# Optimization experiments

Hardware: AMD Instinct MI355X
Metric: run time of the kernel (lower is better)

Reference implementation:

```python
import jax, jax.numpy as jnp
import numpy as np
import math

SQRT32 = math.sqrt(32.0)


def _l2norm(x, eps=1e-12):
    # matches torch.nn.functional.normalize(dim=-1): x / max(||x||, eps)
    n = jnp.linalg.norm(x, axis=-1, keepdims=True)
    return x / jnp.maximum(n, eps)


def setup_inputs() -> dict:
    key = jax.random.key(0)
    k1, k2 = jax.random.split(key)
    z = jax.random.normal(k1, (8, 256, 32, 32), dtype=jnp.float32)
    # trunc_normal_(std=0.02) init approximated by scaled normal
    embed_weight = jax.random.normal(k2, (16384, 256), dtype=jnp.float32) * 0.02
    return {"z": z, "embed_weight": embed_weight}


def reference(z, embed_weight):
    # z: [b, d, h, w] channel-first -> pack to [b*h*w, d]
    b, d, h, w = z.shape
    zf = jnp.transpose(z, (0, 2, 3, 1)).reshape(-1, d)  # [N, d]

    # l2_norm=True, no predefined codebook: distance = -z @ normalize(E)^T
    ew = _l2norm(embed_weight)                          # [K, d]
    dist = -(zf @ ew.T)                                 # [N, K]
    min_encoding_indices = jnp.argmin(dist, axis=1)     # [N]

    # gather UNnormalized embedding rows, then normalize (as in source)
    z_q = _l2norm(embed_weight[min_encoding_indices])   # [N, d]

    # straight-through estimator
    z_q = zf + jax.lax.stop_gradient(z_q - zf)

    loss = jnp.zeros((1,), dtype=z.dtype)

    # unpack to [b, h, w, d]
    zq_bhwd = z_q.reshape(b, h, w, d)
    # torch .long() truncates toward zero; astype(int) does the same
    bit_indices = (zq_bhwd * SQRT32).astype(jnp.int32) + 4
    zq_out = jnp.transpose(zq_bhwd, (0, 3, 1, 2))       # [b, d, h, w]

    return zq_out, min_encoding_indices, bit_indices, loss
```

## Files before the change

### kernel.cpp

```cpp
#include <hip/hip_runtime.h>
#include <math.h>

#define D      256
#define K      16384
#define NPTS   8192
#define DELTA  0.2f
#define LCAP   2048
#define MAXCAP 4000000u

#define O_IDX  2097152
#define O_BIT  2105344
#define O_LOSS 4202496

typedef __attribute__((ext_vector_type(8))) short bf16x8;
typedef __attribute__((ext_vector_type(4))) float f32x4;
typedef unsigned long long u64;

__device__ __forceinline__ unsigned f2s(float f) {
    unsigned u = __float_as_uint(f);
    return (u & 0x80000000u) ? ~u : (u | 0x80000000u);
}
__device__ __forceinline__ float s2f(unsigned s) {
    return __uint_as_float((s & 0x80000000u) ? (s & 0x7fffffffu) : ~s);
}
__device__ __forceinline__ unsigned short f2bf(float f) {
    unsigned u = __float_as_uint(f);
    u += 0x7fffu + ((u >> 16) & 1u);
    return (unsigned short)(u >> 16);
}

__device__ __forceinline__ void gload16(const unsigned short* g, unsigned short* l) {
    __builtin_amdgcn_global_load_lds(
        (const __attribute__((address_space(1))) unsigned int*)g,
        (__attribute__((address_space(3))) unsigned int*)l, 16, 0, 0);
}

__device__ __forceinline__ unsigned lds_off(const void* p) {
    return (unsigned)(size_t)(const __attribute__((address_space(3))) void*)p;
}


__global__ __launch_bounds__(256) void prep(const float* __restrict__ E,
                                            const float* __restrict__ z,
                                            float* __restrict__ den,
                                            unsigned short* __restrict__ ewbT,
                                            unsigned short* __restrict__ zfbT,
                                            float* __restrict__ zf32,
                                            unsigned* __restrict__ gmax,
                                            u64* __restrict__ keys,
                                            unsigned* __restrict__ cnt) {
    const int blk = blockIdx.x, tid = threadIdx.x;
    if (blk < 512) {
        const int lane = tid & 63, wave = tid >> 6;
        if (blk < 32)        gmax[blk * 256 + tid] = 0u;
        else if (blk < 64)   keys[(blk - 32) * 256 + tid] = 0ull;
        else if (blk == 64 && tid < 2) cnt[tid] = 0u;
        #pragma unroll
        for (int j = 0; j < 8; ++j) {
            const int row = blk * 32 + wave * 8 + j;
            const float4 v = *(const float4*)(E + (size_t)row * D + lane * 4);
            float ss = v.x * v.x + v.y * v.y + v.z * v.z + v.w * v.w;
            #pragma unroll
            for (int o = 1; o < 64; o <<= 1) ss += __shfl_xor(ss, o);
            const float dn = fmaxf(sqrtf(ss), 1e-12f);
            const unsigned lo = (unsigned)f2bf(v.x / dn) | ((unsigned)f2bf(v.y / dn) << 16);
            const unsigned hi = (unsigned)f2bf(v.z / dn) | ((unsigned)f2bf(v.w / dn) << 16);
            *(uint2*)(ewbT + ((size_t)(lane >> 1) * K + row) * 8 + (lane & 1) * 4)
                = make_uint2(lo, hi);
            if (lane == 0) den[row] = dn;
        }
    } else {
        const int bi = blk - 512;
        const int b = bi >> 4, hw0 = (bi & 15) * 64;
        __shared__ float t[64][65];
        for (int dc = 0; dc < D; dc += 64) {
            #pragma unroll
            for (int it = 0; it < 16; ++it) {
                const int idx = it * 256 + tid;
                const int dl = idx >> 6, hw = idx & 63;
                t[dl][hw] = z[(size_t)(b * 256 + dc + dl) * 1024 + hw0 + hw];
            }
            __syncthreads();
            #pragma unroll
            for (int it = 0; it < 16; ++it) {
                const int idx = it * 256 + tid;
                const int pl = idx >> 6, dl = idx & 63;
                const float v = t[dl][pl];
                const int p = b * 1024 + hw0 + pl, k = dc + dl;
                zfbT[((size_t)(k >> 3) * NPTS + p) * 8 + (k & 7)] = f2bf(v);
                zf32[(size_t)p * D + k] = v;
            }
            __syncthreads();
        }
    }
}


#define SBAR  __builtin_amdgcn_sched_barrier(0);
#define BARR  __builtin_amdgcn_s_barrier();
#define VMC(N) asm volatile("s_waitcnt vmcnt(" N ")");
#define LGKM_SB  asm volatile("s_waitcnt lgkmcnt(0)"); __builtin_amdgcn_sched_barrier(0);

#define STG_A(slot, t, kk)                                                          \
    do {                                                                            \
        const int cA1_ = (kk) * 4 + hi_, cA2_ = (kk) * 4 + 2 + hi_;                 \
        gload16(zfbT + ((size_t)((t) * 8 + cA1_) * NPTS + m0 + (th_ ^ (cA1_ << 1))) * 8, \
                &sA[slot][cA1_][th_][0]);                                           \
        gload16(zfbT + ((size_t)((t) * 8 + cA2_) * NPTS + m0 + (th_ ^ (cA2_ << 1))) * 8, \
                &sA[slot][cA2_][th_][0]);                                           \
    } while (0)

#define STG_B(slot, t, kk)                                                          \
    do {                                                                            \
        const int cB1_ = (kk) * 4 + hi_, cB2_ = (kk) * 4 + 2 + hi_;                 \
        gload16(ewbT + ((size_t)((t) * 8 + cB1_) * K + n0 + (th_ ^ (cB1_ << 1))) * 8, \
                &sB[slot][cB1_][th_][0]);                                           \
        gload16(ewbT + ((size_t)((t) * 8 + cB2_) * K + n0 + (th_ ^ (cB2_ << 1))) * 8, \
                &sB[slot][cB2_][th_][0]);                                           \
    } while (0)

#define RD_A(slot, kO, mg)                                                          \
    do {                                                                            \
        const unsigned a__ = sAb_ + (unsigned)((slot) * 32768 + (mg) * 1024) + (kO);\
        asm volatile("ds_read_b128 %0, %1"            : "=v"(af_[0]) : "v"(a__));   \
        asm volatile("ds_read_b128 %0, %1 offset:256" : "=v"(af_[1]) : "v"(a__));   \
        asm volatile("ds_read_b128 %0, %1 offset:512" : "=v"(af_[2]) : "v"(a__));   \
        asm volatile("ds_read_b128 %0, %1 offset:768" : "=v"(af_[3]) : "v"(a__));   \
    } while (0)

#define RD_B(slot, kO)                                                              \
    do {                                                                            \
        const unsigned b__ = sBb_ + (unsigned)((slot) * 32768) + (kO);              \
        asm volatile("ds_read_b128 %0, %1"            : "=v"(bf_[0]) : "v"(b__));   \
        asm volatile("ds_read_b128 %0, %1 offset:256" : "=v"(bf_[1]) : "v"(b__));   \
        asm volatile("ds_read_b128 %0, %1 offset:512" : "=v"(bf_[2]) : "v"(b__));   \
        asm volatile("ds_read_b128 %0, %1 offset:768" : "=v"(bf_[3]) : "v"(b__));   \
    } while (0)

#define MF(mg)                                                                      \
    do {                                                                            \
        __builtin_amdgcn_s_setprio(1);                                              \
        _Pragma("unroll")                                                           \
        for (int j_ = 0; j_ < 4; ++j_)                                              \
            _Pragma("unroll")                                                       \
            for (int nt_ = 0; nt_ < 4; ++nt_)                                       \
                acc[(mg) * 4 + j_][nt_] = __builtin_amdgcn_mfma_f32_16x16x32_bf16(  \
                    af_[j_], bf_[nt_], acc[(mg) * 4 + j_][nt_], 0, 0, 0);           \
        __builtin_amdgcn_s_setprio(0);                                              \
    } while (0)

#define KTILE(slot, SA0, SB0, SA1, SB1, V1, V2)                                     \
    RD_A(slot, aOff0_, 0); RD_B(slot, bOff0_); SA0; SBAR BARR LGKM_SB MF(0); SBAR BARR SBAR \
    RD_A(slot, aOff0_, 1);                     SB0; SBAR BARR LGKM_SB MF(1); SBAR VMC(V1) BARR SBAR \
    RD_A(slot, aOff1_, 0); RD_B(slot, bOff1_); SA1; SBAR BARR LGKM_SB MF(0); SBAR BARR SBAR \
    RD_A(slot, aOff1_, 1);                     SB1; SBAR BARR LGKM_SB MF(1); SBAR V2 BARR SBAR

#define GEMM_CORE()                                                                 \
    __shared__ unsigned short sA[2][8][256][8];                                     \
    __shared__ unsigned short sB[2][8][256][8];                                     \
    f32x4 acc[8][4];                                                                \
    _Pragma("unroll")                                                               \
    for (int i_ = 0; i_ < 8; ++i_)                                                  \
        _Pragma("unroll")                                                           \
        for (int j_ = 0; j_ < 4; ++j_) acc[i_][j_] = (f32x4){0.f, 0.f, 0.f, 0.f};   \
    bf16x8 af_[4], bf_[4];                                                          \
    const int th_ = tid & 255, hi_ = tid >> 8;                                      \
    const int aRow_ = wm * 128 + col, bRow_ = wn * 64 + col;                        \
    const unsigned sAb_ = lds_off(&sA[0][0][0][0]);                                 \
    const unsigned sBb_ = lds_off(&sB[0][0][0][0]);                                 \
    const int ck0_ = quad, ck1_ = 4 + quad;                                         \
    const unsigned aOff0_ = (unsigned)((ck0_ * 256 + (aRow_ ^ (ck0_ << 1))) * 16);  \
    const unsigned aOff1_ = (unsigned)((ck1_ * 256 + (aRow_ ^ (ck1_ << 1))) * 16);  \
    const unsigned bOff0_ = (unsigned)((ck0_ * 256 + (bRow_ ^ (ck0_ << 1))) * 16);  \
    const unsigned bOff1_ = (unsigned)((ck1_ * 256 + (bRow_ ^ (ck1_ << 1))) * 16);  \
    STG_A(0, 0, 0); STG_B(0, 0, 0); STG_A(0, 0, 1); STG_B(0, 0, 1);                 \
    SBAR VMC("4") BARR SBAR                                                         \
    KTILE(0, STG_A(1, 1, 0), STG_B(1, 1, 0), STG_A(1, 1, 1), STG_B(1, 1, 1), "4", VMC("4")) \
    KTILE(1, STG_A(0, 2, 0), STG_B(0, 2, 0), STG_A(0, 2, 1), STG_B(0, 2, 1), "4", VMC("4")) \
    KTILE(0, STG_A(1, 3, 0), STG_B(1, 3, 0), STG_A(1, 3, 1), STG_B(1, 3, 1), "4", VMC("4")) \
    KTILE(1, , , , , "0", )

#define CAND_APPEND(e)                                                              \
    do {                                                                            \
        const u64 am_ = __builtin_amdgcn_read_exec();                               \
        const unsigned n_ = (unsigned)__popcll(am_);                                \
        const unsigned rk_ = (unsigned)__popcll(am_ & ((1ull << lane) - 1));        \
        unsigned base_ = 0;                                                         \
        if (rk_ == 0) base_ = atomicAdd(cnt, n_);                                   \
        base_ = (unsigned)__builtin_amdgcn_readfirstlane((int)base_);               \
        const unsigned g_ = base_ + rk_;                                            \
        if (g_ < cap) cand[g_] = (e);                                               \
    } while (0)

#define XCD_DECODE(NT0)                                                             \
    const unsigned bid_ = blockIdx.x;                                               \
    const unsigned j_ = bid_ >> 3;                                                  \
    const int m0 = (int)(((bid_ & 7u) << 2) | (j_ & 3u)) * 256;                     \
    const int n0 = (NT0) + (int)(j_ >> 2) * 256;

__global__ __launch_bounds__(512, 2) void score_seed(const unsigned short* __restrict__ zfbT,
                                                     const unsigned short* __restrict__ ewbT,
                                                     unsigned* __restrict__ gmax,
                                                     u64* __restrict__ cand,
                                                     unsigned* __restrict__ cnt,
                                                     unsigned cap) {
    __shared__ unsigned thrS[256];
    __shared__ u64 lbuf[LCAP];
    __shared__ unsigned lcount, lbase;

    const int tid = threadIdx.x, lane = tid & 63, wave = tid >> 6;
    const int quad = lane >> 4, col = lane & 15;
    const int wm = wave >> 2, wn = wave & 3;
    XCD_DECODE(0)
    const int shsrc = lane & 48;

    if (tid < 256) thrS[tid] = 0u;
    if (tid == 0) lcount = 0u;

    GEMM_CORE()
    __syncthreads();

    float red[8][4];
    #pragma unroll
    for (int mt = 0; mt < 8; ++mt)
        #pragma unroll
        for (int r = 0; r < 4; ++r)
            red[mt][r] = fmaxf(fmaxf(acc[mt][0][r], acc[mt][1][r]),
                               fmaxf(acc[mt][2][r], acc[mt][3][r]));
    #pragma unroll
    for (int off = 1; off < 16; off <<= 1)
        #pragma unroll
        for (int mt = 0; mt < 8; ++mt)
            #pragma unroll
            for (int r = 0; r < 4; ++r)
                red[mt][r] = fmaxf(red[mt][r], __shfl_xor(red[mt][r], off));
    #pragma unroll
    for (int mt = 0; mt < 8; ++mt)
        #pragma unroll
        for (int r = 0; r < 4; ++r) {
            const int pl = wm * 128 + mt * 16 + quad * 4 + r;
            unsigned cur = 0;
            if (col == 0) {
                const unsigned enc = f2s(red[mt][r]);
                const unsigned old = atomicMax(&thrS[pl], enc);
                cur = old > enc ? old : enc;
            }
            cur = (unsigned)__shfl((int)cur, shsrc);
            red[mt][r] = s2f(cur) - DELTA;
        }

    const int ncode0 = n0 + wn * 64 + col;
    #pragma unroll
    for (int mt = 0; mt < 8; ++mt) {
        #pragma unroll
        for (int r = 0; r < 4; ++r) {
            const float tp = red[mt][r];
            const unsigned pt = m0 + wm * 128 + mt * 16 + quad * 4 + r;
            #pragma unroll
            for (int nt = 0; nt < 4; ++nt) {
                const float v = acc[mt][nt][r];
                if (v >= tp) {
                    const unsigned slot = atomicAdd(&lcount, 1u);
                    const u64 e = ((u64)((pt << 14) | (unsigned)(ncode0 + nt * 16)) << 32)
                                  | f2s(v);
                    if (slot < LCAP) lbuf[slot] = e;
                    else CAND_APPEND(e);
                }
            }
        }
    }

    __syncthreads();
    if (tid < 256) atomicMax(&gmax[m0 + tid], thrS[tid]);
    const unsigned m_ = lcount < LCAP ? lcount : LCAP;
    if (tid == 0) lbase = atomicAdd(cnt, m_);
    __syncthreads();
    for (unsigned i = tid; i < m_; i += 512) {
        const unsigned g = lbase + i;
        if (g < cap) cand[g] = lbuf[i];
    }
}

__global__ __launch_bounds__(512, 2) void score_main(const unsigned short* __restrict__ zfbT,
                                                     const unsigned short* __restrict__ ewbT,
                                                     const unsigned* __restrict__ gmax,
                                                     u64* __restrict__ cand,
                                                     unsigned* __restrict__ cnt,
                                                     unsigned cap) {
    __shared__ float thrL[256];
    __shared__ u64 lbuf[LCAP];
    __shared__ unsigned lcount, lbase;

    const int tid = threadIdx.x, lane = tid & 63, wave = tid >> 6;
    const int quad = lane >> 4, col = lane & 15;
    const int wm = wave >> 2, wn = wave & 3;
    XCD_DECODE(2048)

    if (tid < 256) thrL[tid] = s2f(gmax[m0 + tid]) - DELTA;
    if (tid == 0) lcount = 0u;

    GEMM_CORE()
    __syncthreads();

    const int ncode0 = n0 + wn * 64 + col;
    #pragma unroll
    for (int mt = 0; mt < 8; ++mt) {
        #pragma unroll
        for (int r = 0; r < 4; ++r) {
            const int pl = wm * 128 + mt * 16 + quad * 4 + r;
            const float tp = thrL[pl];
            #pragma unroll
            for (int nt = 0; nt < 4; ++nt) {
                const float v = acc[mt][nt][r];
                if (v >= tp) {
                    const unsigned slot = atomicAdd(&lcount, 1u);
                    const u64 e = ((u64)(((unsigned)pl + m0) << 14 | (unsigned)(ncode0 + nt * 16)) << 32)
                                  | f2s(v);
                    if (slot < LCAP) lbuf[slot] = e;
                    else CAND_APPEND(e);
                }
            }
        }
    }

    __syncthreads();
    const unsigned m_ = lcount < LCAP ? lcount : LCAP;
    if (tid == 0) lbase = atomicAdd(cnt, m_);
    __syncthreads();
    for (unsigned i = tid; i < m_; i += 512) {
        const unsigned g = lbase + i;
        if (g < cap) cand[g] = lbuf[i];
    }
}

__global__ __launch_bounds__(256) void cand_max(const u64* __restrict__ cand,
                                                const unsigned* __restrict__ cnt,
                                                unsigned* __restrict__ gmax,
                                                unsigned cap) {
    const unsigned total = min(cnt[0], cap);
    const unsigned stride = gridDim.x * 256;
    for (unsigned i = blockIdx.x * 256 + threadIdx.x; i < total; i += stride) {
        const u64 e = cand[i];
        atomicMax(&gmax[(unsigned)(e >> 46)], (unsigned)(e & 0xffffffffull));
    }
}

__global__ __launch_bounds__(256) void rescore(const float* __restrict__ zf32,
                                               const float* __restrict__ E,
                                               const float* __restrict__ den,
                                               const unsigned* __restrict__ gmax,
                                               const u64* __restrict__ cand,
                                               const unsigned* __restrict__ cnt,
                                               u64* __restrict__ keys,
                                               unsigned cap) {
    const unsigned total = min(cnt[0], cap);
    const int lane = threadIdx.x & 63;
    const unsigned w = (blockIdx.x * 256 + threadIdx.x) >> 6;
    const unsigned nw = gridDim.x * 4;
    for (unsigned base = w * 64; base < total; base += nw * 64) {
        const unsigned i = base + lane;
        u64 e = 0;
        bool keep = false;
        if (i < total) {
            e = cand[i];
            const int p = (int)(e >> 46);
            keep = (s2f((unsigned)(e & 0xffffffffull)) >= s2f(gmax[p]) - DELTA);
        }
        u64 mask = __ballot(keep);
        while (mask) {
            const int src = __ffsll((long long)mask) - 1;
            mask &= mask - 1;
            const unsigned pc = (unsigned)__shfl((int)(unsigned)(e >> 32), src);
            const int p = pc >> 14, c = pc & 16383;
            const float dinv = 1.0f / den[c];
            const float4 a = *(const float4*)(zf32 + (size_t)p * D + lane * 4);
            const float4 b = *(const float4*)(E + (size_t)c * D + lane * 4);
            float sv = fmaf(a.x, b.x * dinv, fmaf(a.y, b.y * dinv,
                       fmaf(a.z, b.z * dinv, a.w * (b.w * dinv))));
            #pragma unroll
            for (int o = 1; o < 64; o <<= 1) sv += __shfl_xor(sv, o);
            if (lane == 0)
                atomicMax(keys + p, ((u64)f2s(sv) << 32) | (unsigned)(16383 - c));
        }
    }
}

__global__ __launch_bounds__(256) void finalize(const float* __restrict__ E,
                                                const float* __restrict__ den,
                                                const u64* __restrict__ keys,
                                                float* __restrict__ out) {
    __shared__ float t[32][257];
    __shared__ int sIdx[32];
    __shared__ float sDen[32];
    const int tid = threadIdx.x;
    const int n0 = blockIdx.x * 32;
    if (tid < 32) {
        const u64 key = keys[n0 + tid];
        const int idx = 16383 - (int)(unsigned)(key & 0xffffffffull);
        sIdx[tid] = idx;
        sDen[tid] = den[idx];
        out[O_IDX + n0 + tid] = (float)idx;
    }
    __syncthreads();
    const float S = 5.65685424949238019520675489683895f;
    #pragma unroll 4
    for (int i = 0; i < 32; ++i) {
        const float v = E[(size_t)sIdx[i] * D + tid] / sDen[i];
        t[i][tid] = v;
        out[O_BIT + (size_t)(n0 + i) * D + tid] = (float)((int)(v * S) + 4);
    }
    __syncthreads();
    const int b = n0 >> 10, hw0 = n0 & 1023;
    const int hwl = tid & 31, cg = tid >> 5;
    #pragma unroll 4
    for (int cc = 0; cc < 32; ++cc) {
        const int c = cc * 8 + cg;
        out[(size_t)(b * 256 + c) * 1024 + hw0 + hwl] = t[hwl][c];
    }
    if (n0 == 0 && tid == 0) out[O_LOSS] = 0.0f;
}

extern "C" void kernel_launch(void* const* d_in, const int* in_sizes, int n_in,
                              void* d_out, int out_size, void* d_ws, size_t ws_size,
                              hipStream_t stream) {
    const float* z = (const float*)d_in[0];
    const float* E = (const float*)d_in[1];
    float* out = (float*)d_out;

    char* w = (char*)d_ws;
    unsigned short* ewbT = (unsigned short*)w;  w += (size_t)K * D * 2;
    unsigned short* zfbT = (unsigned short*)w;  w += (size_t)NPTS * D * 2;
    float*          zf32 = (float*)w;           w += (size_t)NPTS * D * 4;
    u64*            keys = (u64*)w;             w += (size_t)NPTS * 8;
    float*          den  = (float*)w;           w += (size_t)K * 4;
    unsigned*       gmax = (unsigned*)w;        w += (size_t)NPTS * 4;
    unsigned*       cnt  = (unsigned*)w;        w += 256;
    u64*            cand = (u64*)w;
    const size_t fixed = (size_t)(w - (char*)d_ws);
    const size_t avail = ws_size > fixed ? (ws_size - fixed) / 8 : 0;
    const unsigned cap = (unsigned)(avail < (size_t)MAXCAP ? avail : (size_t)MAXCAP);

    prep<<<640, 256, 0, stream>>>(E, z, den, ewbT, zfbT, zf32, gmax, keys, cnt);

    score_seed<<<256, 512, 0, stream>>>(zfbT, ewbT, gmax, cand, cnt, cap);
    score_main<<<1792, 512, 0, stream>>>(zfbT, ewbT, gmax, cand, cnt, cap);

    cand_max<<<256, 256, 0, stream>>>(cand, cnt, gmax, cap);
    rescore<<<1024, 256, 0, stream>>>(zf32, E, den, gmax, cand, cnt, keys, cap);
    finalize<<<NPTS / 32, 256, 0, stream>>>(E, den, keys, out);
}
```

Baseline: 232.9 us.

## Double-buffer MFMA register fragments to overlap LDS reads with matrix math

Splits the A/B register fragments into two sets (a0/a1, b0/b1) and reorganizes the K-tile loop into four phases that issue LDS reads for the next fragment before running MFMAs on the current one. Partial lgkmcnt waits replace full drains, and fewer barriers are used per phase, so LDS latency is meant to hide behind MFMA work. The cost is more VGPRs for the extra fragments, which may lower occupancy, and a more delicate ordering of waits and barriers across buffer slots.

After: 281.3 us. 1.21x slower.

```diff
diff --git a/kernel.cpp b/kernel.cpp
--- a/kernel.cpp
+++ b/kernel.cpp
@@ -99,7 +99,7 @@
 #define SBAR  __builtin_amdgcn_sched_barrier(0);
 #define BARR  __builtin_amdgcn_s_barrier();
 #define VMC(N) asm volatile("s_waitcnt vmcnt(" N ")");
-#define LGKM_SB  asm volatile("s_waitcnt lgkmcnt(0)"); __builtin_amdgcn_sched_barrier(0);
+#define LGKM(N) asm volatile("s_waitcnt lgkmcnt(" N ")"); __builtin_amdgcn_sched_barrier(0);
 
 #define STG_A(slot, t, kk)                                                          \
     do {                                                                            \
@@ -119,25 +119,25 @@
                 &sB[slot][cB2_][th_][0]);                                           \
     } while (0)
 
-#define RD_A(slot, kO, mg)                                                          \
+#define RDA(dst, slot, kO, mg)                                                      \
     do {                                                                            \
         const unsigned a__ = sAb_ + (unsigned)((slot) * 32768 + (mg) * 1024) + (kO);\
-        asm volatile("ds_read_b128 %0, %1"            : "=v"(af_[0]) : "v"(a__));   \
-        asm volatile("ds_read_b128 %0, %1 offset:256" : "=v"(af_[1]) : "v"(a__));   \
-        asm volatile("ds_read_b128 %0, %1 offset:512" : "=v"(af_[2]) : "v"(a__));   \
-        asm volatile("ds_read_b128 %0, %1 offset:768" : "=v"(af_[3]) : "v"(a__));   \
-    } while (0)
-
-#define RD_B(slot, kO)                                                              \
+        asm volatile("ds_read_b128 %0, %1"            : "=v"(dst[0]) : "v"(a__));   \
+        asm volatile("ds_read_b128 %0, %1 offset:256" : "=v"(dst[1]) : "v"(a__));   \
+        asm volatile("ds_read_b128 %0, %1 offset:512" : "=v"(dst[2]) : "v"(a__));   \
+        asm volatile("ds_read_b128 %0, %1 offset:768" : "=v"(dst[3]) : "v"(a__));   \
+    } while (0)
+
+#define RDB(dst, slot, kO)                                                          \
     do {                                                                            \
         const unsigned b__ = sBb_ + (unsigned)((slot) * 32768) + (kO);              \
-        asm volatile("ds_read_b128 %0, %1"            : "=v"(bf_[0]) : "v"(b__));   \
-        asm volatile("ds_read_b128 %0, %1 offset:256" : "=v"(bf_[1]) : "v"(b__));   \
-        asm volatile("ds_read_b128 %0, %1 offset:512" : "=v"(bf_[2]) : "v"(b__));   \
-        asm volatile("ds_read_b128 %0, %1 offset:768" : "=v"(bf_[3]) : "v"(b__));   \
-    } while (0)
-
-#define MF(mg)                                                                      \
+        asm volatile("ds_read_b128 %0, %1"            : "=v"(dst[0]) : "v"(b__));   \
+        asm volatile("ds_read_b128 %0, %1 offset:256" : "=v"(dst[1]) : "v"(b__));   \
+        asm volatile("ds_read_b128 %0, %1 offset:512" : "=v"(dst[2]) : "v"(b__));   \
+        asm volatile("ds_read_b128 %0, %1 offset:768" : "=v"(dst[3]) : "v"(b__));   \
+    } while (0)
+
+#define MF2(mg, A, B)                                                               \
     do {                                                                            \
         __builtin_amdgcn_s_setprio(1);                                              \
         _Pragma("unroll")                                                           \
@@ -145,15 +145,21 @@
             _Pragma("unroll")                                                       \
             for (int nt_ = 0; nt_ < 4; ++nt_)                                       \
                 acc[(mg) * 4 + j_][nt_] = __builtin_amdgcn_mfma_f32_16x16x32_bf16(  \
-                    af_[j_], bf_[nt_], acc[(mg) * 4 + j_][nt_], 0, 0, 0);           \
+                    A[j_], B[nt_], acc[(mg) * 4 + j_][nt_], 0, 0, 0);               \
         __builtin_amdgcn_s_setprio(0);                                              \
     } while (0)
 
-#define KTILE(slot, SA0, SB0, SA1, SB1, V1, V2)                                     \
-    RD_A(slot, aOff0_, 0); RD_B(slot, bOff0_); SA0; SBAR BARR LGKM_SB MF(0); SBAR BARR SBAR \
-    RD_A(slot, aOff0_, 1);                     SB0; SBAR BARR LGKM_SB MF(1); SBAR VMC(V1) BARR SBAR \
-    RD_A(slot, aOff1_, 0); RD_B(slot, bOff1_); SA1; SBAR BARR LGKM_SB MF(0); SBAR BARR SBAR \
-    RD_A(slot, aOff1_, 1);                     SB1; SBAR BARR LGKM_SB MF(1); SBAR V2 BARR SBAR
+#define PH0(s, STG)                                                                 \
+    RDA(a1_, s, aOff0_, 1); STG; SBAR LGKM("4") MF2(0, a0_, b0_); SBAR
+#define PH1(s, STG, VM)                                                             \
+    SBAR VMC(VM) BARR SBAR                                                          \
+    RDA(a0_, s, aOff1_, 0); RDB(b1_, s, bOff1_); STG; SBAR LGKM("8") MF2(1, a1_, b0_); SBAR
+#define PH2(s, STG)                                                                 \
+    RDA(a1_, s, aOff1_, 1); STG; SBAR LGKM("4") MF2(0, a0_, b1_); SBAR
+#define PH3(o, STG)                                                                 \
+    SBAR VMC("2") BARR SBAR                                                         \
+    RDA(a0_, o, aOff0_, 0); RDB(b0_, o, bOff0_); STG; SBAR LGKM("8") MF2(1, a1_, b1_); SBAR \
+    BARR SBAR
 
 #define GEMM_CORE()                                                                 \
     __shared__ unsigned short sA[2][8][256][8];                                     \
@@ -163,7 +169,7 @@
     for (int i_ = 0; i_ < 8; ++i_)                                                  \
         _Pragma("unroll")                                                           \
         for (int j_ = 0; j_ < 4; ++j_) acc[i_][j_] = (f32x4){0.f, 0.f, 0.f, 0.f};   \
-    bf16x8 af_[4], bf_[4];                                                          \
+    bf16x8 a0_[4], a1_[4], b0_[4], b1_[4];                                          \
     const int th_ = tid & 255, hi_ = tid >> 8;                                      \
     const int aRow_ = wm * 128 + col, bRow_ = wn * 64 + col;                        \
     const unsigned sAb_ = lds_off(&sA[0][0][0][0]);                                 \
@@ -173,12 +179,30 @@
     const unsigned aOff1_ = (unsigned)((ck1_ * 256 + (aRow_ ^ (ck1_ << 1))) * 16);  \
     const unsigned bOff0_ = (unsigned)((ck0_ * 256 + (bRow_ ^ (ck0_ << 1))) * 16);  \
     const unsigned bOff1_ = (unsigned)((ck1_ * 256 + (bRow_ ^ (ck1_ << 1))) * 16);  \
+                      \
     STG_A(0, 0, 0); STG_B(0, 0, 0); STG_A(0, 0, 1); STG_B(0, 0, 1);                 \
     SBAR VMC("4") BARR SBAR                                                         \
-    KTILE(0, STG_A(1, 1, 0), STG_B(1, 1, 0), STG_A(1, 1, 1), STG_B(1, 1, 1), "4", VMC("4")) \
-    KTILE(1, STG_A(0, 2, 0), STG_B(0, 2, 0), STG_A(0, 2, 1), STG_B(0, 2, 1), "4", VMC("4")) \
-    KTILE(0, STG_A(1, 3, 0), STG_B(1, 3, 0), STG_A(1, 3, 1), STG_B(1, 3, 1), "4", VMC("4")) \
-    KTILE(1, , , , , "0", )
+    RDA(a0_, 0, aOff0_, 0); RDB(b0_, 0, bOff0_); SBAR                               \
+                                                 \
+    PH0(0, STG_A(1, 1, 0))                                                          \
+    PH1(0, STG_B(1, 1, 0), "2")                                                     \
+    PH2(0, STG_A(1, 1, 1))                                                          \
+    PH3(1, STG_B(1, 1, 1))                                                          \
+                                                 \
+    PH0(1, STG_A(0, 2, 0))                                                          \
+    PH1(1, STG_B(0, 2, 0), "2")                                                     \
+    PH2(1, STG_A(0, 2, 1))                                                          \
+    PH3(0, STG_B(0, 2, 1))                                                          \
+                                                 \
+    PH0(0, STG_A(1, 3, 0))                                                          \
+    PH1(0, STG_B(1, 3, 0), "2")                                                     \
+    PH2(0, STG_A(1, 3, 1))                                                          \
+    PH3(1, STG_B(1, 3, 1))                                                          \
+                                                 \
+    PH0(1, )                                                                        \
+    PH1(1, , "0")                                                                   \
+    PH2(1, )                                                                        \
+    SBAR LGKM("0") MF2(1, a1_, b1_); SBAR
 
 #define CAND_APPEND(e)                                                              \
     do {                                                                            \
```
